# Performance work log

Measured on AMD Instinct MI355X. Metric: run time of the kernel, lower is better.

The kernel has to match this reference:

```python
import jax, jax.numpy as jnp
import numpy as np

SHAPES = ((100, 100), (50, 50), (25, 25))  # (H_l, W_l) per level
D, HEADS, HD, L, P = 256, 8, 32, 3, 4


def setup_inputs() -> dict:
    key = jax.random.key(0)
    ks = jax.random.split(key, 12)
    B = 2
    Nq = sum(h * w for h, w in SHAPES)  # 13125
    inp = {
        "query": jax.random.normal(ks[0], (B, Nq, D), jnp.float32),
        "reference_points": jax.random.uniform(ks[1], (B, Nq, L, 2), jnp.float32),
        "value0": jax.random.normal(ks[2], (B, SHAPES[0][0] * SHAPES[0][1], D), jnp.float32),
        "value1": jax.random.normal(ks[3], (B, SHAPES[1][0] * SHAPES[1][1], D), jnp.float32),
        "value2": jax.random.normal(ks[4], (B, SHAPES[2][0] * SHAPES[2][1], D), jnp.float32),
        "W_val": jax.random.normal(ks[5], (D, D), jnp.float32) * 0.05,
        "b_val": jnp.zeros((D,), jnp.float32),
        "W_off": jax.random.normal(ks[6], (D, HEADS * L * P * 2), jnp.float32) * 0.01,
        "b_off": jax.random.normal(ks[7], (HEADS * L * P * 2,), jnp.float32) * 2.0,
        "W_attn": jax.random.normal(ks[8], (D, HEADS * L * P), jnp.float32) * 0.02,
        "b_attn": jnp.zeros((HEADS * L * P,), jnp.float32),
        "W_out": jax.random.normal(ks[9], (D, D), jnp.float32) * 0.05,
        "b_out": jnp.zeros((D,), jnp.float32),
    }
    return inp


def _bilinear_sample(v, Hl, Wl, loc):
    """v: (B, heads, Hl*Wl, hd); loc: (B, Nq, heads, P, 2) normalized coords in [0,1].
    Matches torch F.grid_sample(mode='bilinear', padding_mode='zeros', align_corners=False)
    applied to grid = 2*loc - 1. Returns (B, Nq, heads, P, hd)."""
    B, heads, _, hd = v.shape
    Nq, Pn = loc.shape[1], loc.shape[3]
    # align_corners=False: pixel = ((g+1)*size - 1)/2 with g = 2*loc-1  ->  loc*size - 0.5
    x = loc[..., 0] * Wl - 0.5
    y = loc[..., 1] * Hl - 0.5
    x0 = jnp.floor(x)
    y0 = jnp.floor(y)
    wx1 = x - x0
    wy1 = y - y0
    out = jnp.zeros((B, Nq, heads, Pn, hd), v.dtype)
    for xi, wx in ((x0, 1.0 - wx1), (x0 + 1.0, wx1)):
        for yi, wy in ((y0, 1.0 - wy1), (y0 + 1.0, wy1)):
            inb = (xi >= 0) & (xi < Wl) & (yi >= 0) & (yi < Hl)
            idx = (jnp.clip(yi, 0, Hl - 1) * Wl + jnp.clip(xi, 0, Wl - 1)).astype(jnp.int32)
            idx_t = idx.transpose(0, 2, 1, 3).reshape(B, heads, Nq * Pn)  # (B,H,Nq*P)
            g = jnp.take_along_axis(v, idx_t[..., None], axis=2)  # (B,H,Nq*P,hd)
            g = g.reshape(B, heads, Nq, Pn, hd).transpose(0, 2, 1, 3, 4)
            w = (wx * wy * inb).astype(v.dtype)  # (B,Nq,heads,P)
            out = out + g * w[..., None]
    return out


def _forward(query, reference_points, values, W_val, b_val, W_off, b_off, W_attn, b_attn, W_out, b_out):
    B, Nq, _ = query.shape
    offs = (query @ W_off + b_off).reshape(B, Nq, HEADS, L, P, 2)
    attn = jax.nn.softmax((query @ W_attn + b_attn).reshape(B, Nq, HEADS, L * P), axis=-1)
    attn = attn.reshape(B, Nq, HEADS, L, P)
    out = jnp.zeros((B, Nq, HEADS, HD), query.dtype)
    for lvl, (Hl, Wl) in enumerate(SHAPES):
        # project values, split heads: (B, heads, H*W, hd)
        v = (values[lvl] @ W_val + b_val).reshape(B, Hl * Wl, HEADS, HD).transpose(0, 2, 1, 3)
        norm = jnp.array([Wl, Hl], query.dtype)
        loc = reference_points[:, :, lvl][:, :, None, None, :] + offs[:, :, :, lvl] / norm  # (B,Nq,heads,P,2)
        sampled = _bilinear_sample(v, Hl, Wl, loc)  # (B,Nq,heads,P,hd)
        out = out + jnp.einsum('bnhp,bnhpd->bnhd', attn[:, :, :, lvl], sampled)
    out = out.reshape(B, Nq, D)
    return out @ W_out + b_out  # dropout is identity at eval


def reference(query, reference_points, value0, value1, value2, W_val, b_val, W_off, b_off, W_attn, b_attn, W_out, b_out):
    return _forward(query, reference_points, (value0, value1, value2), W_val, b_val, W_off, b_off, W_attn, b_attn, W_out, b_out)
```

## Files before the change

kernel.cpp:

```cpp
#include <hip/hip_runtime.h>
#include <hip/hip_bf16.h>
#include <math.h>

#define BATCH 2
#define NQ    13125
#define MQ    26250
#define DM    256
#define NH    8
#define HDIM  32
#define NL    3
#define NP    4
#define NTOK  13125

typedef __attribute__((ext_vector_type(8))) short bf16x8;
typedef __attribute__((ext_vector_type(4))) float f32x4;

__device__ __forceinline__ short f2bf(float f) {
    unsigned u = __float_as_uint(f);
    unsigned r = (u + 0x7FFFu + ((u >> 16) & 1u)) >> 16;
    return (short)r;
}
__device__ __forceinline__ float bf2f(unsigned short u) {
    return __uint_as_float((unsigned)u << 16);
}

__device__ __forceinline__ void gld_lds16(const short* g, short* l) {
    __builtin_amdgcn_global_load_lds(
        (const __attribute__((address_space(1))) unsigned int*)g,
        (__attribute__((address_space(3))) unsigned int*)l, 16, 0, 0);
}

__global__ __launch_bounds__(256) void prep_kernel(const float* __restrict__ Wv,
                                                   const float* __restrict__ Wo,
                                                   const float* __restrict__ Wa,
                                                   const float* __restrict__ Wu,
                                                   const float* __restrict__ q,
                                                   const float* __restrict__ v0,
                                                   const float* __restrict__ v1,
                                                   const float* __restrict__ v2,
                                                   short* __restrict__ Wt,
                                                   short* __restrict__ qb,
                                                   short* __restrict__ vcat)
{
    const int bid = blockIdx.x;
    const int tid = threadIdx.x;
    if (bid < 1280) {
        const int w  = bid >> 8;
        const int Ns[5]   = {256, 192, 96, 256, 96};
        const int Offs[5] = {0, 65536, 114688, 163840, 139264};
        const int N = Ns[w];
        const int flat = (bid & 255) * 256 + tid;
        const int n = flat >> 8, k = flat & 255;
        if (n >= N) return;
        if (w == 4) { Wt[139264 + n * 256 + k] = 0; return; }
        const float* W = (w == 0) ? Wv : ((w == 1) ? Wo : ((w == 2) ? Wa : Wu));
        Wt[Offs[w] + n * 256 + k] = f2bf(W[k * N + n]);
    } else {
        const int i_flat = (bid - 1280) * 256 + tid;
        int i, t;
        if (i_flat < 1680000)      { t = 0; i = i_flat; }
        else if (i_flat < 2960000) { t = 1; i = i_flat - 1680000; }
        else if (i_flat < 3280000) { t = 2; i = i_flat - 2960000; }
        else                       { t = 3; i = i_flat - 3280000; }
        const int row = i >> 6, c = i & 63;
        const float* src = (t == 0) ? q : ((t == 1) ? v0 : ((t == 2) ? v1 : v2));
        int orow;
        short* dst;
        if (t == 0)      { orow = row;                                        dst = qb; }
        else if (t == 1) { orow = (row / 10000) * NTOK + (row % 10000);       dst = vcat; }
        else if (t == 2) { orow = (row / 2500) * NTOK + 10000 + (row % 2500); dst = vcat; }
        else             { orow = (row / 625) * NTOK + 12500 + (row % 625);   dst = vcat; }
        float4 v = ((const float4*)src)[i];
        short4 o;
        o.x = f2bf(v.x); o.y = f2bf(v.y); o.z = f2bf(v.z); o.w = f2bf(v.w);
        ((short4*)dst)[orow * 64 + c] = o;
    }
}

__device__ __forceinline__ void gemm_core128(const short* __restrict__ A,
                                             const short* __restrict__ Wt,
                                             int m0, int n0,
                                             f32x4 (&acc)[4][4],
                                             short* As, short* Bs)
{
    const int tid  = threadIdx.x;
    const int lane = tid & 63;
    const int wave = tid >> 6;
    const int wm   = (wave & 1) * 64;
    const int wn   = (wave >> 1) * 64;
    const int ml   = lane & 15;
    const int kq   = lane >> 4;

    const int row0 = tid >> 2;
    const int row1 = row0 + 64;
    const int kqs  = (tid & 3) ^ ((row0 >> 1) & 3);
    const short* gA0 = A  + (size_t)(m0 + row0) * 256 + kqs * 8;
    const short* gA1 = A  + (size_t)(m0 + row1) * 256 + kqs * 8;
    const short* gB0 = Wt + (size_t)(n0 + row0) * 256 + kqs * 8;
    const short* gB1 = Wt + (size_t)(n0 + row1) * 256 + kqs * 8;
    short* lA0 = As + tid * 8;
    short* lA1 = As + (256 + tid) * 8;
    short* lB0 = Bs + tid * 8;
    short* lB1 = Bs + (256 + tid) * 8;
    const bool a0ok = (m0 + row0) < MQ;
    const bool a1ok = (m0 + row1) < MQ;

    for (int k0 = 0; k0 < 256; k0 += 32) {
        if (a0ok) gld_lds16(gA0 + k0, lA0);
        if (a1ok) gld_lds16(gA1 + k0, lA1);
        gld_lds16(gB0 + k0, lB0);
        gld_lds16(gB1 + k0, lB1);
        __syncthreads();

        bf16x8 af[4], bfr[4];
#pragma unroll
        for (int ti = 0; ti < 4; ++ti) {
            const int r = wm + ti * 16 + ml;
            af[ti] = *(const bf16x8*)&As[r * 32 + ((kq ^ ((r >> 1) & 3)) << 3)];
        }
#pragma unroll
        for (int tj = 0; tj < 4; ++tj) {
            const int r = wn + tj * 16 + ml;
            bfr[tj] = *(const bf16x8*)&Bs[r * 32 + ((kq ^ ((r >> 1) & 3)) << 3)];
        }
#pragma unroll
        for (int ti = 0; ti < 4; ++ti)
#pragma unroll
            for (int tj = 0; tj < 4; ++tj)
                acc[ti][tj] = __builtin_amdgcn_mfma_f32_16x16x32_bf16(af[ti], bfr[tj], acc[ti][tj], 0, 0, 0);

        __syncthreads();
    }
}

__global__ __launch_bounds__(256) void gemm5_kernel(const short* __restrict__ vcat,
                                                    const short* __restrict__ qbf,
                                                    const short* __restrict__ Wt_val,
                                                    const short* __restrict__ Wt_off,
                                                    const float* __restrict__ b_val,
                                                    const float* __restrict__ b_off,
                                                    const float* __restrict__ b_attn,
                                                    short* __restrict__ vws,
                                                    float* __restrict__ offs,
                                                    float* __restrict__ lgts)
{
    __shared__ short As[128 * 32];
    __shared__ short Bs[128 * 32];

    const int y   = blockIdx.y;
    const int m0  = blockIdx.x * 128;
    const bool isv = (y < 2);
    const short* A  = isv ? vcat : qbf;
    const short* Wt = isv ? Wt_val : Wt_off;
    const int n0 = isv ? y * 128 : (y - 2) * 128;

    f32x4 acc[4][4] = {};
    gemm_core128(A, Wt, m0, n0, acc, As, Bs);

    const int tid  = threadIdx.x;
    const int lane = tid & 63;
    const int wave = tid >> 6;
    const int wm   = (wave & 1) * 64;
    const int wn   = (wave >> 1) * 64;
    const int ml   = lane & 15;
    const int kq   = lane >> 4;

#pragma unroll
    for (int tj = 0; tj < 4; ++tj) {
        const int gn = n0 + wn + tj * 16 + ml;
#pragma unroll
        for (int ti = 0; ti < 4; ++ti) {
#pragma unroll
            for (int r = 0; r < 4; ++r) {
                const int gm = m0 + wm + ti * 16 + kq * 4 + r;
                if (gm >= MQ) continue;
                const float v = acc[ti][tj][r];
                if (isv) {
                    vws[(size_t)gm * 256 + gn] = f2bf(v + b_val[gn]);
                } else {
                    if (gn < 192)      offs[(size_t)gm * 192 + gn]        = v + b_off[gn];
                    else if (gn < 288) lgts[(size_t)gm * 96 + (gn - 192)] = v + b_attn[gn - 192];
                }
            }
        }
    }
}

__global__ __launch_bounds__(256) void ogemm_kernel(const short* __restrict__ A,
                                                    const short* __restrict__ Wt,
                                                    const float* __restrict__ bias,
                                                    float* __restrict__ C)
{
    __shared__ short As[128 * 32];
    __shared__ short Bs[128 * 32];
    const int m0 = blockIdx.y * 128;
    const int n0 = blockIdx.x * 128;

    f32x4 acc[4][4] = {};
    gemm_core128(A, Wt, m0, n0, acc, As, Bs);

    const int tid  = threadIdx.x;
    const int lane = tid & 63;
    const int wave = tid >> 6;
    const int wm   = (wave & 1) * 64;
    const int wn   = (wave >> 1) * 64;
    const int ml   = lane & 15;
    const int kq   = lane >> 4;

#pragma unroll
    for (int tj = 0; tj < 4; ++tj) {
        const int gn = n0 + wn + tj * 16 + ml;
#pragma unroll
        for (int ti = 0; ti < 4; ++ti) {
#pragma unroll
            for (int r = 0; r < 4; ++r) {
                const int gm = m0 + wm + ti * 16 + kq * 4 + r;
                if (gm >= MQ) continue;
                C[(size_t)gm * 256 + gn] = acc[ti][tj][r] + bias[gn];
            }
        }
    }
}

__global__ __launch_bounds__(256) void sample_kernel(const short* __restrict__ vws,
                                                     const float* __restrict__ offs,
                                                     const float* __restrict__ logits,
                                                     const float* __restrict__ refp,
                                                     short* __restrict__ mid)
{
    const int q0  = blockIdx.x * 4;
    const int tid = threadIdx.x;

    __shared__ float  s_lg[4][96];
    __shared__ float  s_ref[4][6];
    __shared__ float  s_stat[4][NH][2];
    __shared__ float4 s_w[4][96];
    __shared__ int4   s_i[4][96];

    for (int idx = tid; idx < 384; idx += 256) {
        const int qq = idx / 96, s = idx % 96;
        const int q = q0 + qq;
        if (q < MQ) s_lg[qq][s] = logits[(size_t)q * 96 + s];
    }
    if (tid < 24) {
        const int qq = tid / 6, j = tid % 6;
        const int q = q0 + qq;
        if (q < MQ) s_ref[qq][j] = refp[(size_t)q * 6 + j];
    }
    __syncthreads();

    if (tid < 32) {
        const int qq = tid >> 3, h = tid & 7;
        if (q0 + qq < MQ) {
            float mx = -1e30f;
#pragma unroll
            for (int i = 0; i < 12; ++i) mx = fmaxf(mx, s_lg[qq][h * 12 + i]);
            float ssum = 0.f;
#pragma unroll
            for (int i = 0; i < 12; ++i) ssum += expf(s_lg[qq][h * 12 + i] - mx);
            s_stat[qq][h][0] = mx;
            s_stat[qq][h][1] = 1.f / ssum;
        }
    }
    __syncthreads();

    for (int idx = tid; idx < 384; idx += 256) {
        const int qq = idx / 96, s = idx % 96;
        const int q  = q0 + qq;
        if (q >= MQ) continue;
        const int b  = q / NQ;
        const int h  = s / 12, i = s % 12;
        const int l  = i >> 2, p = i & 3;

        const int Hs[3] = {100, 50, 25};
        const int Wz[3] = {100, 50, 25};
        const int Lo[3] = {0, 10000, 12500};
        const int Wl = Wz[l], Hl = Hs[l];
        const float fW = (float)Wl, fH = (float)Hl;

        const float aw = expf(s_lg[qq][s] - s_stat[qq][h][0]) * s_stat[qq][h][1];

        const int oi = (((h * NL) + l) * NP + p) * 2;
        const float2 offp = *(const float2*)(offs + (size_t)q * 192 + oi);
        const float rx = s_ref[qq][l * 2 + 0];
        const float ry = s_ref[qq][l * 2 + 1];

        const float x = (rx + offp.x / fW) * fW - 0.5f;
        const float y = (ry + offp.y / fH) * fH - 0.5f;
        const float x0f = floorf(x), y0f = floorf(y);
        const int   x0 = (int)x0f,  y0 = (int)y0f;
        const float wx1 = x - x0f, wy1 = y - y0f;
        const float wx0 = 1.f - wx1, wy0 = 1.f - wy1;

        const bool xin0 = (x0 >= 0) && (x0 < Wl);
        const bool xin1 = (x0 + 1 >= 0) && (x0 + 1 < Wl);
        const bool yin0 = (y0 >= 0) && (y0 < Hl);
        const bool yin1 = (y0 + 1 >= 0) && (y0 + 1 < Hl);

        const int cx0 = min(max(x0, 0), Wl - 1);
        const int cx1 = min(max(x0 + 1, 0), Wl - 1);
        const int cy0 = min(max(y0, 0), Hl - 1);
        const int cy1 = min(max(y0 + 1, 0), Hl - 1);

        const int base = b * NTOK + Lo[l];
        int4 idxv;
        idxv.x = base + cy0 * Wl + cx0;
        idxv.y = base + cy0 * Wl + cx1;
        idxv.z = base + cy1 * Wl + cx0;
        idxv.w = base + cy1 * Wl + cx1;

        float4 w;
        w.x = (xin0 && yin0) ? aw * wx0 * wy0 : 0.f;
        w.y = (xin1 && yin0) ? aw * wx1 * wy0 : 0.f;
        w.z = (xin0 && yin1) ? aw * wx0 * wy1 : 0.f;
        w.w = (xin1 && yin1) ? aw * wx1 * wy1 : 0.f;

        s_w[qq][s] = w;
        s_i[qq][s] = idxv;
    }
    __syncthreads();

    {
        const int qq = tid >> 6;
        const int q  = q0 + qq;
        if (q < MQ) {
            const int r  = tid & 63;
            const int h  = r >> 3;
            const int c4 = (r & 7) * 4;
            const int ch = h * HDIM + c4;

            float a0 = 0.f, a1 = 0.f, a2 = 0.f, a3 = 0.f;
#pragma unroll
            for (int s = 0; s < 12; ++s) {
                const float4 w  = s_w[qq][h * 12 + s];
                const int4   id = s_i[qq][h * 12 + s];
                const ushort4 u0 = *(const ushort4*)(vws + (size_t)id.x * DM + ch);
                const ushort4 u1 = *(const ushort4*)(vws + (size_t)id.y * DM + ch);
                const ushort4 u2 = *(const ushort4*)(vws + (size_t)id.z * DM + ch);
                const ushort4 u3 = *(const ushort4*)(vws + (size_t)id.w * DM + ch);
                a0 += w.x * bf2f(u0.x) + w.y * bf2f(u1.x) + w.z * bf2f(u2.x) + w.w * bf2f(u3.x);
                a1 += w.x * bf2f(u0.y) + w.y * bf2f(u1.y) + w.z * bf2f(u2.y) + w.w * bf2f(u3.y);
                a2 += w.x * bf2f(u0.z) + w.y * bf2f(u1.z) + w.z * bf2f(u2.z) + w.w * bf2f(u3.z);
                a3 += w.x * bf2f(u0.w) + w.y * bf2f(u1.w) + w.z * bf2f(u2.w) + w.w * bf2f(u3.w);
            }
            short4 o;
            o.x = f2bf(a0); o.y = f2bf(a1); o.z = f2bf(a2); o.w = f2bf(a3);
            *(short4*)(mid + (size_t)q * DM + ch) = o;
        }
    }
}

extern "C" void kernel_launch(void* const* d_in, const int* in_sizes, int n_in,
                              void* d_out, int out_size, void* d_ws, size_t ws_size,
                              hipStream_t stream)
{
    const float* query  = (const float*)d_in[0];
    const float* refp   = (const float*)d_in[1];
    const float* v0     = (const float*)d_in[2];
    const float* v1     = (const float*)d_in[3];
    const float* v2     = (const float*)d_in[4];
    const float* W_val  = (const float*)d_in[5];
    const float* b_val  = (const float*)d_in[6];
    const float* W_off  = (const float*)d_in[7];
    const float* b_off  = (const float*)d_in[8];
    const float* W_attn = (const float*)d_in[9];
    const float* b_attn = (const float*)d_in[10];
    const float* W_out  = (const float*)d_in[11];
    const float* b_out  = (const float*)d_in[12];
    float* out = (float*)d_out;

    float* ws   = (float*)d_ws;
    float* offs = ws;
    float* lgts = offs + (size_t)MQ * 192;
    short* vws  = (short*)(lgts + (size_t)MQ * 96);
    short* mid  = vws + (size_t)MQ * DM;
    short* qbf  = mid + (size_t)MQ * DM;
    short* vcat = qbf + (size_t)MQ * DM;
    short* Wt   = vcat + (size_t)MQ * DM;
    short* Wt_val = Wt;
    short* Wt_off = Wt + 65536;
    short* Wt_out = Wt + 163840;

    prep_kernel<<<1280 + 13125, 256, 0, stream>>>(W_val, W_off, W_attn, W_out,
                                                  query, v0, v1, v2, Wt, qbf, vcat);
    {
        dim3 grid((MQ + 127) / 128, 5);
        gemm5_kernel<<<grid, 256, 0, stream>>>(vcat, qbf, Wt_val, Wt_off,
                                               b_val, b_off, b_attn, vws, offs, lgts);
    }
    sample_kernel<<<(MQ + 3) / 4, 256, 0, stream>>>(vws, offs, lgts, refp, mid);
    {
        dim3 grid(2, (MQ + 127) / 128);
        ogemm_kernel<<<grid, 256, 0, stream>>>(mid, Wt_out, b_out, out);
    }
}
```

Baseline: 228.7 us.

## Fuse fp32-to-bf16 input conversion into projection GEMM A-tile loads

Removes the separate conversion of query and value tensors to bf16 and instead loads fp32 rows directly inside the projection GEMM, converting to bf16 while writing the A tile into LDS with the same swizzle. The weight-transpose prep becomes its own small kernel. This eliminates a full write and reread of bf16 copies of the activations. In exchange, each N-block of the GEMM rereads the fp32 rows, and the A loads become synchronous register loads instead of async global-to-LDS copies.

```diff
diff --git a/kernel.cpp b/kernel.cpp
--- a/kernel.cpp
+++ b/kernel.cpp
@@ -30,50 +30,139 @@
         (__attribute__((address_space(3))) unsigned int*)l, 16, 0, 0);
 }
 
-__global__ __launch_bounds__(256) void prep_kernel(const float* __restrict__ Wv,
-                                                   const float* __restrict__ Wo,
-                                                   const float* __restrict__ Wa,
-                                                   const float* __restrict__ Wu,
-                                                   const float* __restrict__ q,
-                                                   const float* __restrict__ v0,
-                                                   const float* __restrict__ v1,
-                                                   const float* __restrict__ v2,
-                                                   short* __restrict__ Wt,
-                                                   short* __restrict__ qb,
-                                                   short* __restrict__ vcat)
+__global__ __launch_bounds__(256) void wprep_kernel(const float* __restrict__ Wv,
+                                                    const float* __restrict__ Wo,
+                                                    const float* __restrict__ Wa,
+                                                    const float* __restrict__ Wu,
+                                                    short* __restrict__ Wt)
 {
     const int bid = blockIdx.x;
-    const int tid = threadIdx.x;
-    if (bid < 1280) {
-        const int w  = bid >> 8;
-        const int Ns[5]   = {256, 192, 96, 256, 96};
-        const int Offs[5] = {0, 65536, 114688, 163840, 139264};
-        const int N = Ns[w];
-        const int flat = (bid & 255) * 256 + tid;
-        const int n = flat >> 8, k = flat & 255;
-        if (n >= N) return;
-        if (w == 4) { Wt[139264 + n * 256 + k] = 0; return; }
-        const float* W = (w == 0) ? Wv : ((w == 1) ? Wo : ((w == 2) ? Wa : Wu));
-        Wt[Offs[w] + n * 256 + k] = f2bf(W[k * N + n]);
+    const int w  = bid >> 8;
+    const int Ns[5]   = {256, 192, 96, 256, 96};
+    const int Offs[5] = {0, 65536, 114688, 163840, 139264};
+    const int N = Ns[w];
+    const int flat = (bid & 255) * 256 + threadIdx.x;
+    const int n = flat >> 8, k = flat & 255;
+    if (n >= N) return;
+    if (w == 4) { Wt[139264 + n * 256 + k] = 0; return; }
+    const float* W = (w == 0) ? Wv : ((w == 1) ? Wo : ((w == 2) ? Wa : Wu));
+    Wt[Offs[w] + n * 256 + k] = f2bf(W[k * N + n]);
+}
+
+__global__ __launch_bounds__(256) void gemm5_kernel(const float* __restrict__ query,
+                                                    const float* __restrict__ v0,
+                                                    const float* __restrict__ v1,
+                                                    const float* __restrict__ v2,
+                                                    const short* __restrict__ Wt_val,
+                                                    const short* __restrict__ Wt_off,
+                                                    const float* __restrict__ b_val,
+                                                    const float* __restrict__ b_off,
+                                                    const float* __restrict__ b_attn,
+                                                    short* __restrict__ vws,
+                                                    float* __restrict__ offs,
+                                                    float* __restrict__ lgts)
+{
+    __shared__ short As[128 * 32];
+    __shared__ short Bs[128 * 32];
+
+    const int tid  = threadIdx.x;
+    const int y    = blockIdx.y;
+    const int m0   = blockIdx.x * 128;
+    const bool isv = (y < 2);
+    const short* Wt = isv ? Wt_val : Wt_off;
+    const int n0 = isv ? y * 128 : (y - 2) * 128;
+
+    const int r  = tid >> 1;
+    const int h  = tid & 1;
+    const int gm = m0 + r;
+    const int gmc = (gm < MQ) ? gm : (MQ - 1);
+    const float* Arow;
+    if (isv) {
+        const int b  = gmc / NTOK;
+        const int rr = gmc % NTOK;
+        if (rr < 10000)      Arow = v0 + (size_t)(b * 10000 + rr) * 256;
+        else if (rr < 12500) Arow = v1 + (size_t)(b * 2500 + rr - 10000) * 256;
+        else                 Arow = v2 + (size_t)(b * 625 + rr - 12500) * 256;
     } else {
-        const int i_flat = (bid - 1280) * 256 + tid;
-        int i, t;
-        if (i_flat < 1680000)      { t = 0; i = i_flat; }
-        else if (i_flat < 2960000) { t = 1; i = i_flat - 1680000; }
-        else if (i_flat < 3280000) { t = 2; i = i_flat - 2960000; }
-        else                       { t = 3; i = i_flat - 3280000; }
-        const int row = i >> 6, c = i & 63;
-        const float* src = (t == 0) ? q : ((t == 1) ? v0 : ((t == 2) ? v1 : v2));
-        int orow;
-        short* dst;
-        if (t == 0)      { orow = row;                                        dst = qb; }
-        else if (t == 1) { orow = (row / 10000) * NTOK + (row % 10000);       dst = vcat; }
-        else if (t == 2) { orow = (row / 2500) * NTOK + 10000 + (row % 2500); dst = vcat; }
-        else             { orow = (row / 625) * NTOK + 12500 + (row % 625);   dst = vcat; }
-        float4 v = ((const float4*)src)[i];
-        short4 o;
-        o.x = f2bf(v.x); o.y = f2bf(v.y); o.z = f2bf(v.z); o.w = f2bf(v.w);
-        ((short4*)dst)[orow * 64 + c] = o;
+        Arow = query + (size_t)gmc * 256;
+    }
+    const int pA0 = ((h * 2 + 0) ^ ((r >> 1) & 3)) << 3;
+    const int pA1 = ((h * 2 + 1) ^ ((r >> 1) & 3)) << 3;
+    short* lAr = As + r * 32;
+
+    const int row0 = tid >> 2;
+    const int row1 = row0 + 64;
+    const int kqs  = (tid & 3) ^ ((row0 >> 1) & 3);
+    const short* gB0 = Wt + (size_t)(n0 + row0) * 256 + kqs * 8;
+    const short* gB1 = Wt + (size_t)(n0 + row1) * 256 + kqs * 8;
+    short* lB0 = Bs + tid * 8;
+    short* lB1 = Bs + (256 + tid) * 8;
+
+    const int lane = tid & 63;
+    const int wave = tid >> 6;
+    const int wm   = (wave & 1) * 64;
+    const int wn   = (wave >> 1) * 64;
+    const int ml   = lane & 15;
+    const int kq   = lane >> 4;
+
+    f32x4 acc[4][4] = {};
+
+    for (int k0 = 0; k0 < 256; k0 += 32) {
+        gld_lds16(gB0 + k0, lB0);
+        gld_lds16(gB1 + k0, lB1);
+
+        const float4 a0 = *(const float4*)(Arow + k0 + h * 16 + 0);
+        const float4 a1 = *(const float4*)(Arow + k0 + h * 16 + 4);
+        const float4 a2 = *(const float4*)(Arow + k0 + h * 16 + 8);
+        const float4 a3 = *(const float4*)(Arow + k0 + h * 16 + 12);
+        union { bf16x8 v; short s[8]; } t0, t1;
+        t0.s[0] = f2bf(a0.x); t0.s[1] = f2bf(a0.y); t0.s[2] = f2bf(a0.z); t0.s[3] = f2bf(a0.w);
+        t0.s[4] = f2bf(a1.x); t0.s[5] = f2bf(a1.y); t0.s[6] = f2bf(a1.z); t0.s[7] = f2bf(a1.w);
+        t1.s[0] = f2bf(a2.x); t1.s[1] = f2bf(a2.y); t1.s[2] = f2bf(a2.z); t1.s[3] = f2bf(a2.w);
+        t1.s[4] = f2bf(a3.x); t1.s[5] = f2bf(a3.y); t1.s[6] = f2bf(a3.z); t1.s[7] = f2bf(a3.w);
+        *(bf16x8*)(lAr + pA0) = t0.v;
+        *(bf16x8*)(lAr + pA1) = t1.v;
+
+        __syncthreads();
+
+        bf16x8 af[4], bfr[4];
+#pragma unroll
+        for (int ti = 0; ti < 4; ++ti) {
+            const int rr = wm + ti * 16 + ml;
+            af[ti] = *(const bf16x8*)&As[rr * 32 + ((kq ^ ((rr >> 1) & 3)) << 3)];
+        }
+#pragma unroll
+        for (int tj = 0; tj < 4; ++tj) {
+            const int rr = wn + tj * 16 + ml;
+            bfr[tj] = *(const bf16x8*)&Bs[rr * 32 + ((kq ^ ((rr >> 1) & 3)) << 3)];
+        }
+#pragma unroll
+        for (int ti = 0; ti < 4; ++ti)
+#pragma unroll
+            for (int tj = 0; tj < 4; ++tj)
+                acc[ti][tj] = __builtin_amdgcn_mfma_f32_16x16x32_bf16(af[ti], bfr[tj], acc[ti][tj], 0, 0, 0);
+
+        __syncthreads();
+    }
+
+#pragma unroll
+    for (int tj = 0; tj < 4; ++tj) {
+        const int gn = n0 + wn + tj * 16 + ml;
+#pragma unroll
+        for (int ti = 0; ti < 4; ++ti) {
+#pragma unroll
+            for (int rr = 0; rr < 4; ++rr) {
+                const int gmo = m0 + wm + ti * 16 + kq * 4 + rr;
+                if (gmo >= MQ) continue;
+                const float v = acc[ti][tj][rr];
+                if (isv) {
+                    vws[(size_t)gmo * 256 + gn] = f2bf(v + b_val[gn]);
+                } else {
+                    if (gn < 192)      offs[(size_t)gmo * 192 + gn]        = v + b_off[gn];
+                    else if (gn < 288) lgts[(size_t)gmo * 96 + (gn - 192)] = v + b_attn[gn - 192];
+                }
+            }
+        }
     }
 }
 
@@ -130,59 +219,6 @@
                 acc[ti][tj] = __builtin_amdgcn_mfma_f32_16x16x32_bf16(af[ti], bfr[tj], acc[ti][tj], 0, 0, 0);
 
         __syncthreads();
-    }
-}
-
-__global__ __launch_bounds__(256) void gemm5_kernel(const short* __restrict__ vcat,
-                                                    const short* __restrict__ qbf,
-                                                    const short* __restrict__ Wt_val,
-                                                    const short* __restrict__ Wt_off,
-                                                    const float* __restrict__ b_val,
-                                                    const float* __restrict__ b_off,
-                                                    const float* __restrict__ b_attn,
-                                                    short* __restrict__ vws,
-                                                    float* __restrict__ offs,
-                                                    float* __restrict__ lgts)
-{
-    __shared__ short As[128 * 32];
-    __shared__ short Bs[128 * 32];
-
-    const int y   = blockIdx.y;
-    const int m0  = blockIdx.x * 128;
-    const bool isv = (y < 2);
-    const short* A  = isv ? vcat : qbf;
-    const short* Wt = isv ? Wt_val : Wt_off;
-    const int n0 = isv ? y * 128 : (y - 2) * 128;
-
-    f32x4 acc[4][4] = {};
-    gemm_core128(A, Wt, m0, n0, acc, As, Bs);
-
-    const int tid  = threadIdx.x;
-    const int lane = tid & 63;
-    const int wave = tid >> 6;
-    const int wm   = (wave & 1) * 64;
-    const int wn   = (wave >> 1) * 64;
-    const int ml   = lane & 15;
-    const int kq   = lane >> 4;
-
-#pragma unroll
-    for (int tj = 0; tj < 4; ++tj) {
-        const int gn = n0 + wn + tj * 16 + ml;
-#pragma unroll
-        for (int ti = 0; ti < 4; ++ti) {
-#pragma unroll
-            for (int r = 0; r < 4; ++r) {
-                const int gm = m0 + wm + ti * 16 + kq * 4 + r;
-                if (gm >= MQ) continue;
-                const float v = acc[ti][tj][r];
-                if (isv) {
-                    vws[(size_t)gm * 256 + gn] = f2bf(v + b_val[gn]);
-                } else {
-                    if (gn < 192)      offs[(size_t)gm * 192 + gn]        = v + b_off[gn];
-                    else if (gn < 288) lgts[(size_t)gm * 96 + (gn - 192)] = v + b_attn[gn - 192];
-                }
-            }
-        }
     }
 }
 
@@ -374,18 +410,15 @@
     float* lgts = offs + (size_t)MQ * 192;
     short* vws  = (short*)(lgts + (size_t)MQ * 96);
     short* mid  = vws + (size_t)MQ * DM;
-    short* qbf  = mid + (size_t)MQ * DM;
-    short* vcat = qbf + (size_t)MQ * DM;
-    short* Wt   = vcat + (size_t)MQ * DM;
+    short* Wt   = mid + (size_t)MQ * DM;
     short* Wt_val = Wt;
     short* Wt_off = Wt + 65536;
     short* Wt_out = Wt + 163840;
 
-    prep_kernel<<<1280 + 13125, 256, 0, stream>>>(W_val, W_off, W_attn, W_out,
-                                                  query, v0, v1, v2, Wt, qbf, vcat);
+    wprep_kernel<<<1280, 256, 0, stream>>>(W_val, W_off, W_attn, W_out, Wt);
     {
         dim3 grid((MQ + 127) / 128, 5);
-        gemm5_kernel<<<grid, 256, 0, stream>>>(vcat, qbf, Wt_val, Wt_off,
+        gemm5_kernel<<<grid, 256, 0, stream>>>(query, v0, v1, v2, Wt_val, Wt_off,
                                                b_val, b_off, b_attn, vws, offs, lgts);
     }
     sample_kernel<<<(MQ + 3) / 4, 256, 0, stream>>>(vws, offs, lgts, refp, mid);
```

New measurement: 226.9 us. No clear change (-0.8%).
